# Optimization experiments

Measured on AMD Instinct MI355X. Metric: run time of the kernel, lower is better.

Reference implementation:

```python
import jax, jax.numpy as jnp
import numpy as np

N = 262144   # atoms
G = 8192     # graphs (molecules)
F = 128      # num_features
E = 118      # num_elements
EPS = 1e-6


def setup_inputs() -> dict:
    key = jax.random.key(0)
    k1, k2, k3, k4, k5, k6, k7, k8 = jax.random.split(key, 8)
    z = jax.random.randint(k1, (N,), 0, E)
    elements_one_hot = jax.nn.one_hot(z, E, dtype=jnp.float32)
    psi = jax.random.normal(k2, (G,), dtype=jnp.float32)  # charge / spin per graph (can be negative)
    batch_segments = jnp.sort(jax.random.randint(k3, (N,), 0, G))
    s = 1.0 / np.sqrt(F)
    Wq = jax.random.normal(k4, (F, E), dtype=jnp.float32) * (1.0 / np.sqrt(E))
    Wk = jax.random.normal(k5, (2, F), dtype=jnp.float32) * s
    Wv = jax.random.normal(k6, (2, F), dtype=jnp.float32) * s
    W1 = jax.random.normal(k7, (F, F), dtype=jnp.float32) * s
    W2 = jax.random.normal(k8, (F, F), dtype=jnp.float32) * s
    return {"elements_one_hot": elements_one_hot, "psi": psi, "Wq": Wq, "Wk": Wk,
            "Wv": Wv, "W1": W1, "W2": W2, "batch_segments": batch_segments,
            "num_graphs": G}


def reference(elements_one_hot, psi, Wq, Wk, Wv, W1, W2, batch_segments, num_graphs):
    sqrt_dim = jnp.asarray(np.sqrt(F), dtype=elements_one_hot.dtype)
    # q = Wq(elements_one_hot): [N, F]
    q = elements_one_hot @ Wq.T
    # idx = (psi // inf).int(): 0 for psi >= 0, -1 (-> row 1) for psi < 0
    idx = jnp.where(psi < 0, 1, 0)  # [G]
    k = Wk[idx][batch_segments]  # [N, F]
    v = Wv[idx][batch_segments]  # [N, F]
    q_x_k = jnp.sum(q * k, axis=-1) / sqrt_dim  # [N]
    y = jax.nn.softplus(q_x_k)
    denom = jax.ops.segment_sum(y, batch_segments, num_segments=num_graphs) + EPS  # [G]
    att = psi[batch_segments] * y / denom[batch_segments]  # [N]
    v_att = att[:, None] * v  # [N, F]
    # mlp: SiLU -> Linear(no bias) -> SiLU -> Linear(no bias)
    h = jax.nn.silu(v_att) @ W1.T
    h = jax.nn.silu(h) @ W2.T
    return v_att + h
```

## Files before the change

kernel.cpp:

```cpp
#include <hip/hip_runtime.h>
#include <hip/hip_bf16.h>

#define NATOMS 262144
#define NG     8192
#define FDIM   128
#define NELEM  118
#define EPS    1e-6f
#define TROWS  1024

typedef __attribute__((ext_vector_type(8))) short bf16x8;
typedef __attribute__((ext_vector_type(4))) float f32x4;

__device__ __forceinline__ unsigned short f2bf_rn(float x) {
    unsigned u = __float_as_uint(x);
    unsigned r = (u + 0x7FFFu + ((u >> 16) & 1u)) >> 16;
    return (unsigned short)r;
}
__device__ __forceinline__ float bf2f(unsigned short h) {
    return __uint_as_float((unsigned)h << 16);
}
__device__ __forceinline__ float silu_fast(float v) {
    return v * __builtin_amdgcn_rcpf(1.f + __expf(-v));
}
__device__ __forceinline__ void split2(float x0, float x1,
                                       unsigned& hpack, unsigned& lpack) {
    unsigned u0 = __float_as_uint(x0), u1 = __float_as_uint(x1);
    unsigned h0m = u0 & 0xFFFF0000u, h1m = u1 & 0xFFFF0000u;
    hpack = (u0 >> 16) | h1m;
    float l0 = x0 - __uint_as_float(h0m);
    float l1 = x1 - __uint_as_float(h1m);
    lpack = (__float_as_uint(l0) >> 16) | (__float_as_uint(l1) & 0xFFFF0000u);
}
__device__ __forceinline__ int aoff(int row, int k) {
    return row * FDIM + ((((k >> 3) ^ row) & 15) << 3) + (k & 7);
}

__global__ void prep_kernel(const float* __restrict__ Wq,
                            const float* __restrict__ Wk,
                            const float* __restrict__ W1,
                            const float* __restrict__ W2,
                            float* __restrict__ T,
                            unsigned short* __restrict__ Whi,
                            unsigned short* __restrict__ Wlo,
                            float* __restrict__ denom,
                            unsigned* __restrict__ yminE,
                            unsigned* __restrict__ ymaxE) {
    int b = blockIdx.x, t = threadIdx.x;
    if (b == 0) {
        if (t < 2 * NELEM) {
            int idx = t / NELEM;
            int z   = t - idx * NELEM;
            float dot = 0.f;
            #pragma unroll 8
            for (int f = 0; f < FDIM; ++f)
                dot += Wq[f * NELEM + z] * Wk[idx * FDIM + f];
            float x = dot * 0.08838834764831843f;
            T[t] = fmaxf(x, 0.f) + log1pf(expf(-fabsf(x)));
        }
    } else if (b <= 128) {
        int i = (b - 1) * 256 + t;
        float x = (i < FDIM * FDIM) ? W1[i] : W2[i - FDIM * FDIM];
        unsigned short h = f2bf_rn(x);
        unsigned short l = f2bf_rn(x - bf2f(h));
        Whi[i] = h;
        Wlo[i] = l;
    } else {
        int j = (b - 129) * 256 + t;
        if (j < NG)            denom[j] = 0.f;
        else if (j < 2 * NG)   yminE[j - NG] = 0x7F800000u;
        else                   ymaxE[j - 2 * NG] = 0u;
    }
}

__global__ void zscan_kernel(const float4* __restrict__ onehot4,
                             int* __restrict__ z) {
    const int total4 = NATOMS * NELEM / 4;
    int i = blockIdx.x * blockDim.x + threadIdx.x;
    if (i >= total4) return;
    float4 v = onehot4[i];
    int base = i * 4;
    if (v.x > 0.5f) { int g = base + 0; int n = g / NELEM; z[n] = g - n * NELEM; }
    if (v.y > 0.5f) { int g = base + 1; int n = g / NELEM; z[n] = g - n * NELEM; }
    if (v.z > 0.5f) { int g = base + 2; int n = g / NELEM; z[n] = g - n * NELEM; }
    if (v.w > 0.5f) { int g = base + 3; int n = g / NELEM; z[n] = g - n * NELEM; }
}

__global__ void stat_kernel(const int* __restrict__ seg,
                            const float* __restrict__ psi,
                            const float* __restrict__ T,
                            const int* __restrict__ z,
                            float* __restrict__ y_out,
                            float* __restrict__ denom,
                            unsigned* __restrict__ yminE,
                            unsigned* __restrict__ ymaxE) {
    int n = blockIdx.x * blockDim.x + threadIdx.x;
    int g = seg[n];
    int idx = psi[g] < 0.f ? 1 : 0;
    float yv = T[idx * NELEM + z[n]];
    y_out[n] = yv;

    int lane = threadIdx.x & 63;
    float s = yv, mn = yv, mx = yv;
    #pragma unroll
    for (int d = 1; d < 64; d <<= 1) {
        float os = __shfl_up(s,  (unsigned)d, 64);
        float on = __shfl_up(mn, (unsigned)d, 64);
        float ox = __shfl_up(mx, (unsigned)d, 64);
        int   go = __shfl_up(g,  (unsigned)d, 64);
        if (lane >= d && go == g) {
            s += os;
            mn = fminf(mn, on);
            mx = fmaxf(mx, ox);
        }
    }
    int gn = __shfl_down(g, 1u, 64);
    if (lane == 63 || gn != g) {
        atomicAdd(&denom[g], s);
        atomicMin(&yminE[g], __float_as_uint(mn));
        atomicMax(&ymaxE[g], __float_as_uint(mx));
    }
}

__launch_bounds__(512, 4)
__global__ void mlp_table_kernel(const float* __restrict__ psi_g,
                                 const float* __restrict__ denom,
                                 const unsigned* __restrict__ yminE,
                                 const unsigned* __restrict__ ymaxE,
                                 const float* __restrict__ Wv,
                                 const unsigned short* __restrict__ Whi,
                                 const unsigned short* __restrict__ Wlo,
                                 float* __restrict__ tbl,
                                 float* __restrict__ prm) {
    __shared__ __align__(16) unsigned short Ahi[FDIM * FDIM];
    __shared__ __align__(16) unsigned short Alo[FDIM * FDIM];
    __shared__ float att_s[128];
    __shared__ int   idx_s[128];
    __shared__ float wv_s[2 * FDIM];
    __shared__ float smn[8], smx[8], prm_s[2];

    int t    = threadIdx.x;
    int lane = t & 63;
    int w    = t >> 6;

    {
        float mn = 1e30f, mx = -1e30f;
        for (int j = t; j < NG; j += 512) {
            unsigned me = yminE[j];
            if (me != 0x7F800000u) {
                float r  = __builtin_amdgcn_rcpf(denom[j] + EPS);
                float ps = psi_g[j];
                float a1 = ps * __uint_as_float(me) * r;
                float a2 = ps * __uint_as_float(ymaxE[j]) * r;
                mn = fminf(mn, fminf(a1, a2));
                mx = fmaxf(mx, fmaxf(a1, a2));
            }
        }
        #pragma unroll
        for (int d = 32; d > 0; d >>= 1) {
            mn = fminf(mn, __shfl_xor(mn, d, 64));
            mx = fmaxf(mx, __shfl_xor(mx, d, 64));
        }
        if (lane == 0) { smn[w] = mn; smx[w] = mx; }
        __syncthreads();
        if (t == 0) {
            mn = smn[0]; mx = smx[0];
            #pragma unroll
            for (int q = 1; q < 8; ++q) {
                mn = fminf(mn, smn[q]);
                mx = fmaxf(mx, smx[q]);
            }
            float range = mx - mn;
            if (!(range > 0.f)) range = 1.f;
            prm_s[0] = mn;
            prm_s[1] = range / (float)(TROWS - 1);
            if (blockIdx.x == 0) {
                prm[0] = mn;
                prm[1] = prm_s[1];
                prm[2] = (float)(TROWS - 1) / range;
            }
        }
        __syncthreads();
    }
    float p0 = prm_s[0], hh = prm_s[1];

    int wr   = w >> 2;
    int wc   = w & 3;
    int n0   = blockIdx.x * 128;
    int rbase = wr * 64;
    int jbase = wc * 32;

    if (t < 256) wv_s[t] = Wv[t];
    if (t >= 256 && t < 384) {
        int a = t - 256;
        int n = n0 + a;
        idx_s[a] = n >> 10;
        att_s[a] = p0 + (float)(n & (TROWS - 1)) * hh;
    }
    __syncthreads();

    {
        int a  = t >> 2;
        int kq = (t & 3) * 32;
        float att = att_s[a];
        const float* wvp = &wv_s[idx_s[a] * FDIM + kq];
        #pragma unroll
        for (int kk = 0; kk < 32; kk += 2) {
            float s0 = silu_fast(att * wvp[kk]);
            float s1 = silu_fast(att * wvp[kk + 1]);
            unsigned hp, lp;
            split2(s0, s1, hp, lp);
            int off = aoff(a, kq + kk);
            *(unsigned*)&Ahi[off] = hp;
            *(unsigned*)&Alo[off] = lp;
        }
    }
    __syncthreads();

    int lrow = lane & 15;
    int k0   = (lane >> 4) * 8;

    f32x4 acc[4][2];

    #pragma unroll
    for (int L = 0; L < 2; ++L) {
        const unsigned short* WH = Whi + L * FDIM * FDIM;
        const unsigned short* WL = Wlo + L * FDIM * FDIM;

        #pragma unroll
        for (int mt = 0; mt < 4; ++mt)
            #pragma unroll
            for (int jt = 0; jt < 2; ++jt)
                acc[mt][jt] = (f32x4){0.f, 0.f, 0.f, 0.f};

        #pragma unroll
        for (int kt = 0; kt < 4; ++kt) {
            bf16x8 bh[2], bl[2];
            #pragma unroll
            for (int jt = 0; jt < 2; ++jt) {
                int j = jbase + jt * 16 + lrow;
                bh[jt] = *(const bf16x8*)&WH[j * FDIM + kt * 32 + k0];
                bl[jt] = *(const bf16x8*)&WL[j * FDIM + kt * 32 + k0];
            }
            #pragma unroll
            for (int mt = 0; mt < 4; ++mt) {
                int off = aoff(rbase + mt * 16 + lrow, kt * 32 + k0);
                bf16x8 ah = *(const bf16x8*)&Ahi[off];
                bf16x8 al = *(const bf16x8*)&Alo[off];
                #pragma unroll
                for (int jt = 0; jt < 2; ++jt) {
                    acc[mt][jt] = __builtin_amdgcn_mfma_f32_16x16x32_bf16(ah, bh[jt], acc[mt][jt], 0, 0, 0);
                    acc[mt][jt] = __builtin_amdgcn_mfma_f32_16x16x32_bf16(ah, bl[jt], acc[mt][jt], 0, 0, 0);
                    acc[mt][jt] = __builtin_amdgcn_mfma_f32_16x16x32_bf16(al, bh[jt], acc[mt][jt], 0, 0, 0);
                }
            }
        }

        if (L == 0) {
            __syncthreads();
            #pragma unroll
            for (int mt = 0; mt < 4; ++mt)
                #pragma unroll
                for (int jt = 0; jt < 2; ++jt)
                    #pragma unroll
                    for (int r = 0; r < 4; ++r) {
                        int row = rbase + mt * 16 + (lane >> 4) * 4 + r;
                        int col = jbase + jt * 16 + lrow;
                        float s = silu_fast(acc[mt][jt][r]);
                        unsigned u = __float_as_uint(s);
                        unsigned hm = u & 0xFFFF0000u;
                        float l = s - __uint_as_float(hm);
                        int off = aoff(row, col);
                        Ahi[off] = (unsigned short)(u >> 16);
                        Alo[off] = (unsigned short)(__float_as_uint(l) >> 16);
                    }
            __syncthreads();
        }
    }

    #pragma unroll
    for (int mt = 0; mt < 4; ++mt)
        #pragma unroll
        for (int jt = 0; jt < 2; ++jt) {
            int row0 = rbase + mt * 16 + (lane >> 4) * 4;
            int col  = jbase + jt * 16 + lrow;
            float* p = tbl + (long)(n0 + row0) * FDIM + col;
            #pragma unroll
            for (int r = 0; r < 4; ++r) {
                int row = row0 + r;
                float vatt = att_s[row] * wv_s[idx_s[row] * FDIM + col];
                p[r * FDIM] = acc[mt][jt][r] + vatt;
            }
        }
}

__global__ void interp_kernel(const int* __restrict__ seg,
                              const float* __restrict__ psi,
                              const float* __restrict__ y,
                              const float* __restrict__ denom,
                              const float* __restrict__ prm,
                              const float* __restrict__ tbl,
                              float* __restrict__ out) {
    const int total = NATOMS * 32;
    float p0 = prm[0], p2 = prm[2];
    int stride = gridDim.x * blockDim.x;
    for (int i = blockIdx.x * blockDim.x + threadIdx.x; i < total; i += stride) {
        int n  = i >> 5;
        int jq = i & 31;
        int g  = seg[n];
        float att = psi[g] * y[n] * __builtin_amdgcn_rcpf(denom[g] + EPS);
        int idx = psi[g] < 0.f ? 1 : 0;
        float x = (att - p0) * p2;
        int b = (int)floorf(x);
        b = min(max(b, 0), TROWS - 2);
        float t = x - (float)b;
        const f32x4* r0 = (const f32x4*)&tbl[(long)((idx << 10) + b) * FDIM];
        f32x4 a = r0[jq];
        f32x4 c = r0[jq + 32];
        f32x4 o;
        o.x = a.x + t * (c.x - a.x);
        o.y = a.y + t * (c.y - a.y);
        o.z = a.z + t * (c.z - a.z);
        o.w = a.w + t * (c.w - a.w);
        __builtin_nontemporal_store(o, (f32x4*)&out[(long)n * FDIM + jq * 4]);
    }
}

extern "C" void kernel_launch(void* const* d_in, const int* in_sizes, int n_in,
                              void* d_out, int out_size, void* d_ws, size_t ws_size,
                              hipStream_t stream) {
    const float* onehot = (const float*)d_in[0];
    const float* psi    = (const float*)d_in[1];
    const float* Wq     = (const float*)d_in[2];
    const float* Wk     = (const float*)d_in[3];
    const float* Wv     = (const float*)d_in[4];
    const float* W1     = (const float*)d_in[5];
    const float* W2     = (const float*)d_in[6];
    const int*   seg    = (const int*)d_in[7];
    float*       out    = (float*)d_out;

    char* ws = (char*)d_ws;
    float*          denom = (float*)ws;
    unsigned*       yminE = (unsigned*)(ws + 32768);
    unsigned*       ymaxE = (unsigned*)(ws + 65536);
    float*          T     = (float*)(ws + 98304);
    float*          prm   = (float*)(ws + 99328);
    unsigned short* Whi   = (unsigned short*)(ws + 100352);
    unsigned short* Wlo   = (unsigned short*)(ws + 165888);
    float*          y     = (float*)(ws + 231424);
    int*            z     = (int*)(ws + 231424 + NATOMS * 4);
    float*          tbl   = (float*)(ws + 231424 + NATOMS * 4);

    prep_kernel<<<225, 256, 0, stream>>>(Wq, Wk, W1, W2, T, Whi, Wlo,
                                         denom, yminE, ymaxE);

    {
        const int total4 = NATOMS * NELEM / 4;
        zscan_kernel<<<(total4 + 255) / 256, 256, 0, stream>>>((const float4*)onehot, z);
    }

    stat_kernel<<<NATOMS / 256, 256, 0, stream>>>(seg, psi, T, z, y,
                                                  denom, yminE, ymaxE);

    mlp_table_kernel<<<2 * TROWS / 128, 512, 0, stream>>>(psi, denom, yminE, ymaxE,
                                                          Wv, Whi, Wlo, tbl, prm);

    interp_kernel<<<4096, 256, 0, stream>>>(seg, psi, y, denom, prm, tbl, out);
}
```

Before: 82.09 us.

## Fuse one-hot scan with y/stat pass and split weights inside MLP kernel

Merges the element-index scan and the per-atom softplus/segment-stat pass into one kernel, where a 32-lane group reads one atom's one-hot row and reduces the index with shuffles. Per-block segment sums, mins and maxes are combined serially by one thread before the atomics. The bf16 hi/lo split of W1/W2 moves out of prep into the MLP table kernel, computed on the fly from fp32 loads, which removes a kernel launch and the intermediate z and weight buffers. Tradeoffs: more atomics, since 8-atom blocks aggregate less than 64-lane wave scans, and some redundant split work inside the MFMA loop.

```diff
diff --git a/kernel.cpp b/kernel.cpp
--- a/kernel.cpp
+++ b/kernel.cpp
@@ -11,14 +11,6 @@
 typedef __attribute__((ext_vector_type(8))) short bf16x8;
 typedef __attribute__((ext_vector_type(4))) float f32x4;
 
-__device__ __forceinline__ unsigned short f2bf_rn(float x) {
-    unsigned u = __float_as_uint(x);
-    unsigned r = (u + 0x7FFFu + ((u >> 16) & 1u)) >> 16;
-    return (unsigned short)r;
-}
-__device__ __forceinline__ float bf2f(unsigned short h) {
-    return __uint_as_float((unsigned)h << 16);
-}
 __device__ __forceinline__ float silu_fast(float v) {
     return v * __builtin_amdgcn_rcpf(1.f + __expf(-v));
 }
@@ -37,11 +29,7 @@
 
 __global__ void prep_kernel(const float* __restrict__ Wq,
                             const float* __restrict__ Wk,
-                            const float* __restrict__ W1,
-                            const float* __restrict__ W2,
                             float* __restrict__ T,
-                            unsigned short* __restrict__ Whi,
-                            unsigned short* __restrict__ Wlo,
                             float* __restrict__ denom,
                             unsigned* __restrict__ yminE,
                             unsigned* __restrict__ ymaxE) {
@@ -57,67 +45,71 @@
             float x = dot * 0.08838834764831843f;
             T[t] = fmaxf(x, 0.f) + log1pf(expf(-fabsf(x)));
         }
-    } else if (b <= 128) {
-        int i = (b - 1) * 256 + t;
-        float x = (i < FDIM * FDIM) ? W1[i] : W2[i - FDIM * FDIM];
-        unsigned short h = f2bf_rn(x);
-        unsigned short l = f2bf_rn(x - bf2f(h));
-        Whi[i] = h;
-        Wlo[i] = l;
     } else {
-        int j = (b - 129) * 256 + t;
+        int j = (b - 1) * 256 + t;
         if (j < NG)            denom[j] = 0.f;
-        else if (j < 2 * NG)   yminE[j - NG] = 0x7F800000u;
-        else                   ymaxE[j - 2 * NG] = 0u;
-    }
-}
-
-__global__ void zscan_kernel(const float4* __restrict__ onehot4,
-                             int* __restrict__ z) {
-    const int total4 = NATOMS * NELEM / 4;
-    int i = blockIdx.x * blockDim.x + threadIdx.x;
-    if (i >= total4) return;
-    float4 v = onehot4[i];
-    int base = i * 4;
-    if (v.x > 0.5f) { int g = base + 0; int n = g / NELEM; z[n] = g - n * NELEM; }
-    if (v.y > 0.5f) { int g = base + 1; int n = g / NELEM; z[n] = g - n * NELEM; }
-    if (v.z > 0.5f) { int g = base + 2; int n = g / NELEM; z[n] = g - n * NELEM; }
-    if (v.w > 0.5f) { int g = base + 3; int n = g / NELEM; z[n] = g - n * NELEM; }
-}
-
-__global__ void stat_kernel(const int* __restrict__ seg,
-                            const float* __restrict__ psi,
-                            const float* __restrict__ T,
-                            const int* __restrict__ z,
-                            float* __restrict__ y_out,
-                            float* __restrict__ denom,
-                            unsigned* __restrict__ yminE,
-                            unsigned* __restrict__ ymaxE) {
-    int n = blockIdx.x * blockDim.x + threadIdx.x;
+        else if (j < 2 * NG)   ymaxE[j - NG] = 0u;
+        else                   yminE[j - 2 * NG] = 0xFFFFFFFFu;
+    }
+}
+
+__global__ void zy_stat_kernel(const float* __restrict__ onehot,
+                               const int* __restrict__ seg,
+                               const float* __restrict__ psi,
+                               const float* __restrict__ T,
+                               float* __restrict__ y_out,
+                               float* __restrict__ denom,
+                               unsigned* __restrict__ yminE,
+                               unsigned* __restrict__ ymaxE) {
+    __shared__ int   gS[8];
+    __shared__ float yS[8];
+
+    int t   = threadIdx.x;
+    int grp = t >> 5;
+    int l   = t & 31;
+    int n   = blockIdx.x * 8 + grp;
+
+    const float* row = onehot + (long)n * NELEM;
+    float v0 = row[l];
+    float v1 = row[l + 32];
+    float v2 = row[l + 64];
+    float v3 = (l < NELEM - 96) ? row[l + 96] : 0.f;
+
+    int zc = -1;
+    if (v0 > 0.5f) zc = l;
+    if (v1 > 0.5f) zc = l + 32;
+    if (v2 > 0.5f) zc = l + 64;
+    if (v3 > 0.5f) zc = l + 96;
+    #pragma unroll
+    for (int d = 16; d > 0; d >>= 1)
+        zc = max(zc, __shfl_xor(zc, d, 32));
+
     int g = seg[n];
     int idx = psi[g] < 0.f ? 1 : 0;
-    float yv = T[idx * NELEM + z[n]];
-    y_out[n] = yv;
-
-    int lane = threadIdx.x & 63;
-    float s = yv, mn = yv, mx = yv;
-    #pragma unroll
-    for (int d = 1; d < 64; d <<= 1) {
-        float os = __shfl_up(s,  (unsigned)d, 64);
-        float on = __shfl_up(mn, (unsigned)d, 64);
-        float ox = __shfl_up(mx, (unsigned)d, 64);
-        int   go = __shfl_up(g,  (unsigned)d, 64);
-        if (lane >= d && go == g) {
-            s += os;
-            mn = fminf(mn, on);
-            mx = fmaxf(mx, ox);
-        }
-    }
-    int gn = __shfl_down(g, 1u, 64);
-    if (lane == 63 || gn != g) {
-        atomicAdd(&denom[g], s);
-        atomicMin(&yminE[g], __float_as_uint(mn));
-        atomicMax(&ymaxE[g], __float_as_uint(mx));
+    float yv = T[idx * NELEM + zc];
+    if (l == 0) {
+        y_out[n] = yv;
+        gS[grp] = g;
+        yS[grp] = yv;
+    }
+    __syncthreads();
+
+    if (t == 0) {
+        int i = 0;
+        while (i < 8) {
+            int gg = gS[i];
+            float s = yS[i], mn = yS[i], mx = yS[i];
+            int j = i + 1;
+            while (j < 8 && gS[j] == gg) {
+                float v = yS[j];
+                s += v; mn = fminf(mn, v); mx = fmaxf(mx, v);
+                ++j;
+            }
+            atomicAdd(&denom[gg], s);
+            atomicMin(&yminE[gg], __float_as_uint(mn));
+            atomicMax(&ymaxE[gg], __float_as_uint(mx));
+            i = j;
+        }
     }
 }
 
@@ -127,8 +119,8 @@
                                  const unsigned* __restrict__ yminE,
                                  const unsigned* __restrict__ ymaxE,
                                  const float* __restrict__ Wv,
-                                 const unsigned short* __restrict__ Whi,
-                                 const unsigned short* __restrict__ Wlo,
+                                 const float* __restrict__ W1,
+                                 const float* __restrict__ W2,
                                  float* __restrict__ tbl,
                                  float* __restrict__ prm) {
     __shared__ __align__(16) unsigned short Ahi[FDIM * FDIM];
@@ -146,7 +138,7 @@
         float mn = 1e30f, mx = -1e30f;
         for (int j = t; j < NG; j += 512) {
             unsigned me = yminE[j];
-            if (me != 0x7F800000u) {
+            if (me != 0xFFFFFFFFu) {
                 float r  = __builtin_amdgcn_rcpf(denom[j] + EPS);
                 float ps = psi_g[j];
                 float a1 = ps * __uint_as_float(me) * r;
@@ -223,8 +215,7 @@
 
     #pragma unroll
     for (int L = 0; L < 2; ++L) {
-        const unsigned short* WH = Whi + L * FDIM * FDIM;
-        const unsigned short* WL = Wlo + L * FDIM * FDIM;
+        const float* Wf = (L == 0) ? W1 : W2;
 
         #pragma unroll
         for (int mt = 0; mt < 4; ++mt)
@@ -238,8 +229,14 @@
             #pragma unroll
             for (int jt = 0; jt < 2; ++jt) {
                 int j = jbase + jt * 16 + lrow;
-                bh[jt] = *(const bf16x8*)&WH[j * FDIM + kt * 32 + k0];
-                bl[jt] = *(const bf16x8*)&WL[j * FDIM + kt * 32 + k0];
+                const float4* wp = (const float4*)&Wf[j * FDIM + kt * 32 + k0];
+                float4 wa = wp[0], wb = wp[1];
+                union { unsigned u[4]; bf16x8 v; } H, L8;
+                split2(wa.x, wa.y, H.u[0], L8.u[0]);
+                split2(wa.z, wa.w, H.u[1], L8.u[1]);
+                split2(wb.x, wb.y, H.u[2], L8.u[2]);
+                split2(wb.z, wb.w, H.u[3], L8.u[3]);
+                bh[jt] = H.v; bl[jt] = L8.v;
             }
             #pragma unroll
             for (int mt = 0; mt < 4; ++mt) {
@@ -339,30 +336,21 @@
     float*       out    = (float*)d_out;
 
     char* ws = (char*)d_ws;
-    float*          denom = (float*)ws;
-    unsigned*       yminE = (unsigned*)(ws + 32768);
-    unsigned*       ymaxE = (unsigned*)(ws + 65536);
-    float*          T     = (float*)(ws + 98304);
-    float*          prm   = (float*)(ws + 99328);
-    unsigned short* Whi   = (unsigned short*)(ws + 100352);
-    unsigned short* Wlo   = (unsigned short*)(ws + 165888);
-    float*          y     = (float*)(ws + 231424);
-    int*            z     = (int*)(ws + 231424 + NATOMS * 4);
-    float*          tbl   = (float*)(ws + 231424 + NATOMS * 4);
-
-    prep_kernel<<<225, 256, 0, stream>>>(Wq, Wk, W1, W2, T, Whi, Wlo,
-                                         denom, yminE, ymaxE);
-
-    {
-        const int total4 = NATOMS * NELEM / 4;
-        zscan_kernel<<<(total4 + 255) / 256, 256, 0, stream>>>((const float4*)onehot, z);
-    }
-
-    stat_kernel<<<NATOMS / 256, 256, 0, stream>>>(seg, psi, T, z, y,
-                                                  denom, yminE, ymaxE);
+    float*    denom = (float*)ws;
+    unsigned* ymaxE = (unsigned*)(ws + 32768);
+    unsigned* yminE = (unsigned*)(ws + 65536);
+    float*    T     = (float*)(ws + 98304);
+    float*    prm   = (float*)(ws + 99328);
+    float*    y     = (float*)(ws + 100352);
+    float*    tbl   = (float*)(ws + 100352 + NATOMS * 4);
+
+    prep_kernel<<<97, 256, 0, stream>>>(Wq, Wk, T, denom, yminE, ymaxE);
+
+    zy_stat_kernel<<<NATOMS / 8, 256, 0, stream>>>(onehot, seg, psi, T, y,
+                                                   denom, yminE, ymaxE);
 
     mlp_table_kernel<<<2 * TROWS / 128, 512, 0, stream>>>(psi, denom, yminE, ymaxE,
-                                                          Wv, Whi, Wlo, tbl, prm);
+                                                          Wv, W1, W2, tbl, prm);
 
     interp_kernel<<<4096, 256, 0, stream>>>(seg, psi, y, denom, prm, tbl, out);
 }
```

New measurement: 105.6 us. +28.7%, slower.

## Fuse zscan with prep, split weights in-kernel, precompute per-graph interp scale

Applied to the files above, without the earlier changes.

Merges the one-hot scan and the parameter prep into a single launch, with each thread loading four float4s using nontemporal loads. The bf16 hi/lo weight split now happens inside the MLP table kernel when each tile is loaded, so the separate prep pass and its workspace are gone. The table kernel also writes a per-graph factor q = psi/denom·p2, which lets the interp kernel compute the table index with one fma and read the sign bit from q instead of loading psi and denom and doing a reciprocal. The min sentinel becomes 0xFFFFFFFF, which is safe because y is a positive softplus value. The cost is redundant split work in every MLP block and fewer, larger scan blocks.

```diff
diff --git a/kernel.cpp b/kernel.cpp
--- a/kernel.cpp
+++ b/kernel.cpp
@@ -7,18 +7,11 @@
 #define NELEM  118
 #define EPS    1e-6f
 #define TROWS  1024
+#define NBLK_SCAN 7552
 
 typedef __attribute__((ext_vector_type(8))) short bf16x8;
 typedef __attribute__((ext_vector_type(4))) float f32x4;
 
-__device__ __forceinline__ unsigned short f2bf_rn(float x) {
-    unsigned u = __float_as_uint(x);
-    unsigned r = (u + 0x7FFFu + ((u >> 16) & 1u)) >> 16;
-    return (unsigned short)r;
-}
-__device__ __forceinline__ float bf2f(unsigned short h) {
-    return __uint_as_float((unsigned)h << 16);
-}
 __device__ __forceinline__ float silu_fast(float v) {
     return v * __builtin_amdgcn_rcpf(1.f + __expf(-v));
 }
@@ -35,54 +28,52 @@
     return row * FDIM + ((((k >> 3) ^ row) & 15) << 3) + (k & 7);
 }
 
-__global__ void prep_kernel(const float* __restrict__ Wq,
-                            const float* __restrict__ Wk,
-                            const float* __restrict__ W1,
-                            const float* __restrict__ W2,
-                            float* __restrict__ T,
-                            unsigned short* __restrict__ Whi,
-                            unsigned short* __restrict__ Wlo,
-                            float* __restrict__ denom,
-                            unsigned* __restrict__ yminE,
-                            unsigned* __restrict__ ymaxE) {
+__global__ void zscan_prep_kernel(const f32x4* __restrict__ onehot4,
+                                  int* __restrict__ z,
+                                  const float* __restrict__ Wq,
+                                  const float* __restrict__ Wk,
+                                  float* __restrict__ T,
+                                  float* __restrict__ denom,
+                                  unsigned* __restrict__ yminE,
+                                  unsigned* __restrict__ ymaxE) {
     int b = blockIdx.x, t = threadIdx.x;
-    if (b == 0) {
-        if (t < 2 * NELEM) {
-            int idx = t / NELEM;
-            int z   = t - idx * NELEM;
-            float dot = 0.f;
-            #pragma unroll 8
-            for (int f = 0; f < FDIM; ++f)
-                dot += Wq[f * NELEM + z] * Wk[idx * FDIM + f];
-            float x = dot * 0.08838834764831843f;
-            T[t] = fmaxf(x, 0.f) + log1pf(expf(-fabsf(x)));
-        }
-    } else if (b <= 128) {
-        int i = (b - 1) * 256 + t;
-        float x = (i < FDIM * FDIM) ? W1[i] : W2[i - FDIM * FDIM];
-        unsigned short h = f2bf_rn(x);
-        unsigned short l = f2bf_rn(x - bf2f(h));
-        Whi[i] = h;
-        Wlo[i] = l;
+    if (b < NBLK_SCAN) {
+        int base = b * 1024 + t;
+        f32x4 v[4];
+        #pragma unroll
+        for (int k = 0; k < 4; ++k)
+            v[k] = __builtin_nontemporal_load(&onehot4[base + k * 256]);
+        #pragma unroll
+        for (int k = 0; k < 4; ++k) {
+            int i4 = (base + k * 256) * 4;
+            #pragma unroll
+            for (int q = 0; q < 4; ++q)
+                if (v[k][q] > 0.5f) {
+                    int gf = i4 + q;
+                    int n  = gf / NELEM;
+                    z[n] = gf - n * NELEM;
+                }
+        }
     } else {
-        int j = (b - 129) * 256 + t;
-        if (j < NG)            denom[j] = 0.f;
-        else if (j < 2 * NG)   yminE[j - NG] = 0x7F800000u;
-        else                   ymaxE[j - 2 * NG] = 0u;
-    }
-}
-
-__global__ void zscan_kernel(const float4* __restrict__ onehot4,
-                             int* __restrict__ z) {
-    const int total4 = NATOMS * NELEM / 4;
-    int i = blockIdx.x * blockDim.x + threadIdx.x;
-    if (i >= total4) return;
-    float4 v = onehot4[i];
-    int base = i * 4;
-    if (v.x > 0.5f) { int g = base + 0; int n = g / NELEM; z[n] = g - n * NELEM; }
-    if (v.y > 0.5f) { int g = base + 1; int n = g / NELEM; z[n] = g - n * NELEM; }
-    if (v.z > 0.5f) { int g = base + 2; int n = g / NELEM; z[n] = g - n * NELEM; }
-    if (v.w > 0.5f) { int g = base + 3; int n = g / NELEM; z[n] = g - n * NELEM; }
+        int pb = b - NBLK_SCAN;
+        if (pb == 0) {
+            if (t < 2 * NELEM) {
+                int idx = t / NELEM;
+                int zz  = t - idx * NELEM;
+                float dot = 0.f;
+                #pragma unroll 8
+                for (int f = 0; f < FDIM; ++f)
+                    dot += Wq[f * NELEM + zz] * Wk[idx * FDIM + f];
+                float x = dot * 0.08838834764831843f;
+                T[t] = fmaxf(x, 0.f) + log1pf(expf(-fabsf(x)));
+            }
+        } else {
+            int j = (pb - 1) * 256 + t;
+            if (j < NG)            denom[j] = 0.f;
+            else if (j < 2 * NG)   ymaxE[j - NG] = 0u;
+            else                   yminE[j - 2 * NG] = 0xFFFFFFFFu;
+        }
+    }
 }
 
 __global__ void stat_kernel(const int* __restrict__ seg,
@@ -127,16 +118,17 @@
                                  const unsigned* __restrict__ yminE,
                                  const unsigned* __restrict__ ymaxE,
                                  const float* __restrict__ Wv,
-                                 const unsigned short* __restrict__ Whi,
-                                 const unsigned short* __restrict__ Wlo,
+                                 const float* __restrict__ W1,
+                                 const float* __restrict__ W2,
                                  float* __restrict__ tbl,
-                                 float* __restrict__ prm) {
+                                 float* __restrict__ prm,
+                                 float* __restrict__ q) {
     __shared__ __align__(16) unsigned short Ahi[FDIM * FDIM];
     __shared__ __align__(16) unsigned short Alo[FDIM * FDIM];
     __shared__ float att_s[128];
     __shared__ int   idx_s[128];
     __shared__ float wv_s[2 * FDIM];
-    __shared__ float smn[8], smx[8], prm_s[2];
+    __shared__ float smn[8], smx[8], prm_s[3];
 
     int t    = threadIdx.x;
     int lane = t & 63;
@@ -146,7 +138,7 @@
         float mn = 1e30f, mx = -1e30f;
         for (int j = t; j < NG; j += 512) {
             unsigned me = yminE[j];
-            if (me != 0x7F800000u) {
+            if (me != 0xFFFFFFFFu) {
                 float r  = __builtin_amdgcn_rcpf(denom[j] + EPS);
                 float ps = psi_g[j];
                 float a1 = ps * __uint_as_float(me) * r;
@@ -165,23 +157,31 @@
         if (t == 0) {
             mn = smn[0]; mx = smx[0];
             #pragma unroll
-            for (int q = 1; q < 8; ++q) {
-                mn = fminf(mn, smn[q]);
-                mx = fmaxf(mx, smx[q]);
+            for (int qq = 1; qq < 8; ++qq) {
+                mn = fminf(mn, smn[qq]);
+                mx = fmaxf(mx, smx[qq]);
             }
             float range = mx - mn;
             if (!(range > 0.f)) range = 1.f;
+            float p2 = (float)(TROWS - 1) / range;
             prm_s[0] = mn;
             prm_s[1] = range / (float)(TROWS - 1);
+            prm_s[2] = p2;
             if (blockIdx.x == 0) {
                 prm[0] = mn;
                 prm[1] = prm_s[1];
-                prm[2] = (float)(TROWS - 1) / range;
+                prm[2] = p2;
+                prm[3] = mn * p2;
             }
         }
         __syncthreads();
     }
-    float p0 = prm_s[0], hh = prm_s[1];
+    float p0 = prm_s[0], hh = prm_s[1], p2 = prm_s[2];
+
+    {
+        int g = blockIdx.x * 512 + t;
+        q[g] = psi_g[g] * __builtin_amdgcn_rcpf(denom[g] + EPS) * p2;
+    }
 
     int wr   = w >> 2;
     int wc   = w & 3;
@@ -223,8 +223,7 @@
 
     #pragma unroll
     for (int L = 0; L < 2; ++L) {
-        const unsigned short* WH = Whi + L * FDIM * FDIM;
-        const unsigned short* WL = Wlo + L * FDIM * FDIM;
+        const float* Wf = (L == 0) ? W1 : W2;
 
         #pragma unroll
         for (int mt = 0; mt < 4; ++mt)
@@ -238,8 +237,14 @@
             #pragma unroll
             for (int jt = 0; jt < 2; ++jt) {
                 int j = jbase + jt * 16 + lrow;
-                bh[jt] = *(const bf16x8*)&WH[j * FDIM + kt * 32 + k0];
-                bl[jt] = *(const bf16x8*)&WL[j * FDIM + kt * 32 + k0];
+                const f32x4* wp = (const f32x4*)&Wf[j * FDIM + kt * 32 + k0];
+                f32x4 wa = wp[0], wb = wp[1];
+                union { unsigned u[4]; bf16x8 v; } H, L8;
+                split2(wa[0], wa[1], H.u[0], L8.u[0]);
+                split2(wa[2], wa[3], H.u[1], L8.u[1]);
+                split2(wb[0], wb[1], H.u[2], L8.u[2]);
+                split2(wb[2], wb[3], H.u[3], L8.u[3]);
+                bh[jt] = H.v; bl[jt] = L8.v;
             }
             #pragma unroll
             for (int mt = 0; mt < 4; ++mt) {
@@ -294,22 +299,21 @@
 }
 
 __global__ void interp_kernel(const int* __restrict__ seg,
-                              const float* __restrict__ psi,
                               const float* __restrict__ y,
-                              const float* __restrict__ denom,
+                              const float* __restrict__ q,
                               const float* __restrict__ prm,
                               const float* __restrict__ tbl,
                               float* __restrict__ out) {
     const int total = NATOMS * 32;
-    float p0 = prm[0], p2 = prm[2];
+    float cB = prm[3];
     int stride = gridDim.x * blockDim.x;
     for (int i = blockIdx.x * blockDim.x + threadIdx.x; i < total; i += stride) {
         int n  = i >> 5;
         int jq = i & 31;
         int g  = seg[n];
-        float att = psi[g] * y[n] * __builtin_amdgcn_rcpf(denom[g] + EPS);
-        int idx = psi[g] < 0.f ? 1 : 0;
-        float x = (att - p0) * p2;
+        float qv = q[g];
+        float x  = fmaf(y[n], qv, -cB);
+        int idx  = (int)(__float_as_uint(qv) >> 31);
         int b = (int)floorf(x);
         b = min(max(b, 0), TROWS - 2);
         float t = x - (float)b;
@@ -317,10 +321,10 @@
         f32x4 a = r0[jq];
         f32x4 c = r0[jq + 32];
         f32x4 o;
-        o.x = a.x + t * (c.x - a.x);
-        o.y = a.y + t * (c.y - a.y);
-        o.z = a.z + t * (c.z - a.z);
-        o.w = a.w + t * (c.w - a.w);
+        o[0] = a[0] + t * (c[0] - a[0]);
+        o[1] = a[1] + t * (c[1] - a[1]);
+        o[2] = a[2] + t * (c[2] - a[2]);
+        o[3] = a[3] + t * (c[3] - a[3]);
         __builtin_nontemporal_store(o, (f32x4*)&out[(long)n * FDIM + jq * 4]);
     }
 }
@@ -339,30 +343,24 @@
     float*       out    = (float*)d_out;
 
     char* ws = (char*)d_ws;
-    float*          denom = (float*)ws;
-    unsigned*       yminE = (unsigned*)(ws + 32768);
-    unsigned*       ymaxE = (unsigned*)(ws + 65536);
-    float*          T     = (float*)(ws + 98304);
-    float*          prm   = (float*)(ws + 99328);
-    unsigned short* Whi   = (unsigned short*)(ws + 100352);
-    unsigned short* Wlo   = (unsigned short*)(ws + 165888);
-    float*          y     = (float*)(ws + 231424);
-    int*            z     = (int*)(ws + 231424 + NATOMS * 4);
-    float*          tbl   = (float*)(ws + 231424 + NATOMS * 4);
-
-    prep_kernel<<<225, 256, 0, stream>>>(Wq, Wk, W1, W2, T, Whi, Wlo,
-                                         denom, yminE, ymaxE);
-
-    {
-        const int total4 = NATOMS * NELEM / 4;
-        zscan_kernel<<<(total4 + 255) / 256, 256, 0, stream>>>((const float4*)onehot, z);
-    }
+    float*    denom = (float*)ws;
+    unsigned* ymaxE = (unsigned*)(ws + 32768);
+    unsigned* yminE = (unsigned*)(ws + 65536);
+    float*    T     = (float*)(ws + 98304);
+    float*    prm   = (float*)(ws + 99328);
+    float*    q     = (float*)(ws + 100352);
+    float*    y     = (float*)(ws + 133120);
+    int*      z     = (int*)(ws + 133120 + NATOMS * 4);
+    float*    tbl   = (float*)(ws + 133120 + NATOMS * 4);
+
+    zscan_prep_kernel<<<NBLK_SCAN + 97, 256, 0, stream>>>(
+        (const f32x4*)onehot, z, Wq, Wk, T, denom, yminE, ymaxE);
 
     stat_kernel<<<NATOMS / 256, 256, 0, stream>>>(seg, psi, T, z, y,
                                                   denom, yminE, ymaxE);
 
     mlp_table_kernel<<<2 * TROWS / 128, 512, 0, stream>>>(psi, denom, yminE, ymaxE,
-                                                          Wv, Whi, Wlo, tbl, prm);
-
-    interp_kernel<<<4096, 256, 0, stream>>>(seg, psi, y, denom, prm, tbl, out);
-}
+                                                          Wv, W1, W2, tbl, prm, q);
+
+    interp_kernel<<<4096, 256, 0, stream>>>(seg, y, q, prm, tbl, out);
+}
```

After: 74.53 us, median of 3. -9.2%, faster.
